# Kernel tuning notes

Measured on AMD Instinct MI355X. Metric: run time of the kernel, lower is better.

## Reference

```python
import jax, jax.numpy as jnp
import numpy as np

N = 524288
H = 128
EPS = 1e-4
SYMP_N = 32  # min(N, 32)
# loss weights from init_kwargs
W_RECON, W_CONS, W_EVO, W_SYMP, W_GAUGE = 1.0, 10.0, 5.0, 0.1, 5.0


def _mlp(x, W1, b1, W2, b2, W3, b3):
    h = jnp.tanh(x @ W1 + b1)
    h = jnp.tanh(h @ W2 + b2)
    return h @ W3 + b3


def _encode(p, q, params):
    out = _mlp(jnp.stack([p, q], axis=-1), *params)  # [N,2]
    return out[:, 0], out[:, 1]


def _decode(P, Q, params):
    out = _mlp(jnp.stack([P, Q], axis=-1), *params)
    return out[:, 0], out[:, 1]


def setup_inputs() -> dict:
    key = jax.random.key(0)
    ks = jax.random.split(key, 24)
    f32 = jnp.float32

    def nrm(k, shape, scale=1.0):
        return (scale * jax.random.normal(k, shape, dtype=f32))

    inp = {
        'p0': nrm(ks[0], (N,)),
        'q0': nrm(ks[1], (N,)),
        'p1': nrm(ks[2], (N,)),
        'q1': nrm(ks[3], (N,)),
        'omega_values': jax.random.uniform(ks[4], (N,), dtype=f32, minval=0.5, maxval=2.0),
        'dt': jnp.asarray(0.05, dtype=f32),
        'P_true': nrm(ks[5], (N,)),
        'Q_true': nrm(ks[6], (N,)),
        # encoder params (2 -> H -> H -> 2), fan-in scaled init
        'enc_W1': nrm(ks[7], (2, H), 1.0 / np.sqrt(2.0)),
        'enc_b1': jnp.zeros((H,), f32),
        'enc_W2': nrm(ks[8], (H, H), 1.0 / np.sqrt(H)),
        'enc_b2': jnp.zeros((H,), f32),
        'enc_W3': nrm(ks[9], (H, 2), 1.0 / np.sqrt(H)),
        'enc_b3': jnp.zeros((2,), f32),
        # decoder params
        'dec_W1': nrm(ks[10], (2, H), 1.0 / np.sqrt(2.0)),
        'dec_b1': jnp.zeros((H,), f32),
        'dec_W2': nrm(ks[11], (H, H), 1.0 / np.sqrt(H)),
        'dec_b2': jnp.zeros((H,), f32),
        'dec_W3': nrm(ks[12], (H, 2), 1.0 / np.sqrt(H)),
        'dec_b3': jnp.zeros((2,), f32),
    }
    return inp


def _loss(p0, q0, p1, q1, omega_values, dt, P_true, Q_true, enc, dec):
    P0, Q0 = _encode(p0, q0, enc)
    P1, Q1 = _encode(p1, q1, enc)
    p0_recon, q0_recon = _decode(P0, Q0, dec)

    recon_loss = jnp.mean((p0 - p0_recon) ** 2 + (q0 - q0_recon) ** 2)
    conservation_loss = jnp.mean((P0 - P1) ** 2)
    evolution_loss = jnp.mean(1.0 - jnp.cos((Q1 - Q0) - omega_values * dt))

    # symplectic loss: batched central finite differences over first 32 samples
    pi, qi = p0[:SYMP_N], q0[:SYMP_N]
    pp = jnp.concatenate([pi + EPS, pi - EPS, pi, pi])          # [4*32]
    qq = jnp.concatenate([qi, qi, qi + EPS, qi - EPS])
    P, Q = _encode(pp, qq, enc)
    P_pp, P_pm, P_qp, P_qm = jnp.split(P, 4)
    Q_pp, Q_pm, Q_qp, Q_qm = jnp.split(Q, 4)
    inv2e = 1.0 / (2.0 * EPS)
    dP_dp = (P_pp - P_pm) * inv2e
    dP_dq = (P_qp - P_qm) * inv2e
    dQ_dp = (Q_pp - Q_pm) * inv2e
    dQ_dq = (Q_qp - Q_qm) * inv2e
    pb = dP_dq * dQ_dp - dP_dp * dQ_dq
    symplectic_loss = jnp.mean((jnp.abs(pb) - 1.0) ** 2)

    gauge_loss = jnp.mean((P0 - P_true) ** 2) + jnp.mean(1.0 - jnp.cos(Q0 - Q_true))

    total = (W_RECON * recon_loss + W_CONS * conservation_loss
             + W_EVO * evolution_loss + W_SYMP * symplectic_loss
             + W_GAUGE * gauge_loss)
    return jnp.stack([total, recon_loss, conservation_loss,
                      evolution_loss, symplectic_loss, gauge_loss])


def reference(p0, q0, p1, q1, omega_values, dt, P_true, Q_true,
              enc_W1, enc_b1, enc_W2, enc_b2, enc_W3, enc_b3,
              dec_W1, dec_b1, dec_W2, dec_b2, dec_W3, dec_b3):
    enc = (enc_W1, enc_b1, enc_W2, enc_b2, enc_W3, enc_b3)
    dec = (dec_W1, dec_b1, dec_W2, dec_b2, dec_W3, dec_b3)
    return _loss(p0, q0, p1, q1, omega_values, dt, P_true, Q_true, enc, dec)
```

## Files before the change

kernel.cpp:

```cpp
#include <hip/hip_runtime.h>
#include <stdint.h>
#include <math.h>


constexpr float EPS_FD = 1e-4f;
constexpr int NBLK = 256;

typedef float f32x4 __attribute__((ext_vector_type(4)));
typedef short s16x8 __attribute__((ext_vector_type(8)));

__device__ __forceinline__ float tanh_fast(float x) {
  float e = __builtin_amdgcn_exp2f(x * 2.8853900817779268f);
  return 1.0f - 2.0f * __builtin_amdgcn_rcpf(e + 1.0f);
}
__device__ __forceinline__ float cos_fast(float x) {
  return __builtin_amdgcn_cosf(x * 0.15915494309189535f);
}
__device__ __forceinline__ unsigned bf16rne(float f) {
  union { float f; unsigned u; } v; v.f = f;
  return (v.u + 0x7FFFu + ((v.u >> 16) & 1u)) >> 16;
}
__device__ __forceinline__ unsigned pack2rne(float a, float b) {
  return bf16rne(a) | (bf16rne(b) << 16);
}
__device__ __forceinline__ unsigned packbf(float lo, float hi) {
  union { float f; unsigned u; } a, b; a.f = lo; b.f = hi;
  return __builtin_amdgcn_perm(b.u + 0x8000u, a.u + 0x8000u, 0x07060302u);
}

template<bool SCAT>
__device__ __forceinline__ void mlp_pass(
    float pe, float qe, unsigned* hrow, const uint4* Bf, const float* epi,
    float w100, float w101, float w110, float w111, float b10, float b11,
    int lane, int quad, int l15, float& vP, float& vQ)
{
#pragma unroll
  for (int ee = 0; ee < 16; ee++) {
    int src = SCAT ? (16 * (ee >> 2) + (ee & 3)) : ee;
    float p = __shfl(pe, src, 64);
    float q = __shfl(qe, src, 64);
    float a0 = tanh_fast(fmaf(p, w100, fmaf(q, w110, b10)));
    float a1 = tanh_fast(fmaf(p, w101, fmaf(q, w111, b11)));
    hrow[ee * 68 + lane] = packbf(a0, a1);
  }
  __builtin_amdgcn_wave_barrier();

  s16x8 A[4];
#pragma unroll
  for (int s = 0; s < 4; s++) {
    uint4 u = *reinterpret_cast<const uint4*>(&hrow[l15 * 68 + 16 * s + 4 * quad]);
    A[s] = *reinterpret_cast<s16x8*>(&u);
  }
  __builtin_amdgcn_wave_barrier();

  f32x4 acc[8];
#pragma unroll
  for (int t = 0; t < 8; t++) {
    float b2v = epi[16 * t + l15];
    f32x4 z = {b2v, b2v, b2v, b2v};
    acc[t] = z;
  }
#pragma unroll
  for (int s = 0; s < 4; s++) {
#pragma unroll
    for (int t = 0; t < 8; t++) {
      uint4 bu = Bf[(s * 8 + t) * 64 + lane];
      s16x8 Bv = *reinterpret_cast<s16x8*>(&bu);
      acc[t] = __builtin_amdgcn_mfma_f32_16x16x32_bf16(A[s], Bv, acc[t], 0, 0, 0);
    }
  }

  float sP[4] = {0, 0, 0, 0}, sQ[4] = {0, 0, 0, 0};
#pragma unroll
  for (int t = 0; t < 8; t++) {
    float w3Pv = epi[128 + 16 * t + l15];
    float w3Qv = epi[256 + 16 * t + l15];
#pragma unroll
    for (int r = 0; r < 4; r++) {
      float h = tanh_fast(acc[t][r]);
      sP[r] = fmaf(h, w3Pv, sP[r]);
      sQ[r] = fmaf(h, w3Qv, sQ[r]);
    }
  }
#pragma unroll
  for (int m = 1; m < 16; m <<= 1) {
#pragma unroll
    for (int r = 0; r < 4; r++) {
      sP[r] += __shfl_xor(sP[r], m, 64);
      sQ[r] += __shfl_xor(sQ[r], m, 64);
    }
  }
  vP = (l15 == 0) ? sP[0] : (l15 == 1) ? sP[1] : (l15 == 2) ? sP[2] : sP[3];
  vQ = (l15 == 0) ? sQ[0] : (l15 == 1) ? sQ[1] : (l15 == 2) ? sQ[2] : sQ[3];
}

__global__ __launch_bounds__(1024, 1) void mlp_main(
    const float* __restrict__ p0, const float* __restrict__ q0,
    const float* __restrict__ p1, const float* __restrict__ q1,
    const float* __restrict__ eW1, const float* __restrict__ eb1,
    const float* __restrict__ eW2, const float* __restrict__ eb2,
    const float* __restrict__ eW3, const float* __restrict__ eb3,
    const float* __restrict__ dW1, const float* __restrict__ db1,
    const float* __restrict__ dW2, const float* __restrict__ db2,
    const float* __restrict__ dW3, const float* __restrict__ db3,
    const float* __restrict__ omega, const float* __restrict__ Pt,
    const float* __restrict__ Qt, const float* __restrict__ dtp,
    float* __restrict__ acc5, unsigned* __restrict__ counter,
    float* __restrict__ PQ, float* __restrict__ out, int n)
{
  __shared__ uint4 BfE[2048];
  __shared__ uint4 BfD[2048];
  __shared__ unsigned h1s[16][16 * 68 + 4];
  __shared__ float encEpi[384];
  __shared__ float decEpi[384];
  __shared__ float red[16][5];
  __shared__ unsigned lastflag;

  int tid = threadIdx.x;
#pragma unroll
  for (int it = 0; it < 8; it++) {
    int id = tid + it * 1024;
    int jj = id & 3, ln = (id >> 2) & 63, f = id >> 8;
    int s = f >> 3, t = f & 7;
    int k   = 32 * s + 8 * (ln >> 4) + 2 * jj;
    int col = 16 * t + (ln & 15);
    ((unsigned*)BfE)[id] = pack2rne(eW2[k * 128 + col], eW2[(k + 1) * 128 + col]);
    ((unsigned*)BfD)[id] = pack2rne(dW2[k * 128 + col], dW2[(k + 1) * 128 + col]);
  }
  if (tid < 128) {
    encEpi[tid]       = eb2[tid];
    encEpi[128 + tid] = eW3[2 * tid];
    encEpi[256 + tid] = eW3[2 * tid + 1];
  } else if (tid < 256) {
    int u = tid - 128;
    decEpi[u]       = db2[u];
    decEpi[128 + u] = dW3[2 * u];
    decEpi[256 + u] = dW3[2 * u + 1];
  }

  int wave = tid >> 6, lane = tid & 63;
  int quad = lane >> 4, l15 = lane & 15;

  float ew100 = eW1[2 * lane],       ew101 = eW1[2 * lane + 1];
  float ew110 = eW1[128 + 2 * lane], ew111 = eW1[128 + 2 * lane + 1];
  float eb10 = eb1[2 * lane], eb11 = eb1[2 * lane + 1];
  float dw100 = dW1[2 * lane],       dw101 = dW1[2 * lane + 1];
  float dw110 = dW1[128 + 2 * lane], dw111 = dW1[128 + 2 * lane + 1];
  float db10 = db1[2 * lane], db11 = db1[2 * lane + 1];
  float eb3P = eb3[0], eb3Q = eb3[1];
  float db3P = db3[0], db3Q = db3[1];
  float dt = dtp[0];
  float s0 = 0.f, s1 = 0.f, s2 = 0.f, s3 = 0.f, s4 = 0.f;
  __syncthreads();

  int nwaves = gridDim.x * 16;
  int gwave  = blockIdx.x * 16 + wave;
  int ntiles = (n + 15) >> 4;
  unsigned* hrow = &h1s[wave][0];

  if (gwave < 128) {
    int r = gwave;
    int m = r & 31, c = r >> 5;
    float p = p0[m], q = q0[m];
    p += (c == 0) ? EPS_FD : (c == 1) ? -EPS_FD : 0.f;
    q += (c == 2) ? EPS_FD : (c == 3) ? -EPS_FD : 0.f;
    float* hf = (float*)hrow;
    int t0 = 2 * lane, t1 = 2 * lane + 1;
    float h0 = tanhf(fmaf(p, eW1[t0], fmaf(q, eW1[128 + t0], eb1[t0])));
    float h1v = tanhf(fmaf(p, eW1[t1], fmaf(q, eW1[128 + t1], eb1[t1])));
    hf[t0] = h0; hf[t1] = h1v;
    __builtin_amdgcn_wave_barrier();
    float a0 = eb2[t0], a1 = eb2[t1];
#pragma unroll 8
    for (int k = 0; k < 128; k++) {
      float hk = hf[k];
      a0 = fmaf(hk, eW2[k * 128 + t0], a0);
      a1 = fmaf(hk, eW2[k * 128 + t1], a1);
    }
    float g0 = tanhf(a0), g1 = tanhf(a1);
    float cP = fmaf(g0, eW3[2 * t0],     g1 * eW3[2 * t1]);
    float cQ = fmaf(g0, eW3[2 * t0 + 1], g1 * eW3[2 * t1 + 1]);
#pragma unroll
    for (int mm = 1; mm < 64; mm <<= 1) {
      cP += __shfl_xor(cP, mm, 64);
      cQ += __shfl_xor(cQ, mm, 64);
    }
    if (lane == 0) {
      atomicExch(&PQ[2 * r],     cP + eb3P);
      atomicExch(&PQ[2 * r + 1], cQ + eb3Q);
    }
    __builtin_amdgcn_wave_barrier();
  }

  for (int tile = gwave; tile < ntiles; tile += nwaves) {
    int base = tile * 16;
    int e = base + l15; if (e >= n) e = n - 1;
    float p0e = p0[e], q0e = q0[e];
    float p1e = p1[e], q1e = q1[e];
    int o = base + quad * 4 + l15;
    int o16 = base + quad * 4 + (l15 & 3);
    if (o16 >= n) o16 = n - 1;
    float Lom = omega[o16], LPt = Pt[o16], LQt = Qt[o16];
    float Lp0 = p0[o16],    Lq0 = q0[o16];

    float P0v, Q0v, P1v, Q1v, RPv, RQv;
    mlp_pass<false>(p0e, q0e, hrow, BfE, encEpi,
                    ew100, ew101, ew110, ew111, eb10, eb11,
                    lane, quad, l15, P0v, Q0v);
    P0v += eb3P; Q0v += eb3Q;
    mlp_pass<false>(p1e, q1e, hrow, BfE, encEpi,
                    ew100, ew101, ew110, ew111, eb10, eb11,
                    lane, quad, l15, P1v, Q1v);
    P1v += eb3P; Q1v += eb3Q;
    mlp_pass<true>(P0v, Q0v, hrow, BfD, decEpi,
                   dw100, dw101, dw110, dw111, db10, db11,
                   lane, quad, l15, RPv, RQv);
    RPv += db3P; RQv += db3Q;

    if (l15 < 4 && o < n) {
      float dp = Lp0 - RPv, dq = Lq0 - RQv;
      s0 += dp * dp + dq * dq;
      float d1 = P0v - P1v; s1 += d1 * d1;
      s2 += 1.0f - cos_fast(Q1v - Q0v - Lom * dt);
      float g = P0v - LPt; s3 += g * g;
      s4 += 1.0f - cos_fast(Q0v - LQt);
    }
  }

#pragma unroll
  for (int m = 1; m < 64; m <<= 1) {
    s0 += __shfl_xor(s0, m, 64);
    s1 += __shfl_xor(s1, m, 64);
    s2 += __shfl_xor(s2, m, 64);
    s3 += __shfl_xor(s3, m, 64);
    s4 += __shfl_xor(s4, m, 64);
  }
  if (lane == 0) {
    red[wave][0] = s0; red[wave][1] = s1; red[wave][2] = s2;
    red[wave][3] = s3; red[wave][4] = s4;
  }
  __syncthreads();
  if (tid == 0) {
#pragma unroll
    for (int i = 0; i < 5; i++) {
      float v = 0.f;
#pragma unroll
      for (int w = 0; w < 16; w++) v += red[w][i];
      atomicAdd(&acc5[i], v);
    }
    __threadfence();
    unsigned prev = atomicAdd(counter, 1u);
    lastflag = (prev == gridDim.x - 1) ? 1u : 0u;
  }
  __syncthreads();
  if (lastflag) {
    __threadfence();
    if (tid < 64) {
      float v = 0.f;
      if (tid < 32) {
        float Ppp = atomicAdd(&PQ[2 * tid], 0.f);
        float Qpp = atomicAdd(&PQ[2 * tid + 1], 0.f);
        float Ppm = atomicAdd(&PQ[2 * (32 + tid)], 0.f);
        float Qpm = atomicAdd(&PQ[2 * (32 + tid) + 1], 0.f);
        float Pqp = atomicAdd(&PQ[2 * (64 + tid)], 0.f);
        float Qqp = atomicAdd(&PQ[2 * (64 + tid) + 1], 0.f);
        float Pqm = atomicAdd(&PQ[2 * (96 + tid)], 0.f);
        float Qqm = atomicAdd(&PQ[2 * (96 + tid) + 1], 0.f);
        float inv2e = 1.0f / (2.0f * EPS_FD);
        float dPdp = (Ppp - Ppm) * inv2e, dPdq = (Pqp - Pqm) * inv2e;
        float dQdp = (Qpp - Qpm) * inv2e, dQdq = (Qqp - Qqm) * inv2e;
        float pb = dPdq * dQdp - dPdp * dQdq;
        float d = fabsf(pb) - 1.0f;
        v = d * d;
      }
#pragma unroll
      for (int m = 1; m < 64; m <<= 1) v += __shfl_xor(v, m, 64);
      if (tid == 0) {
        float inv_n = 1.0f / (float)n;
        float recon = atomicAdd(&acc5[0], 0.f) * inv_n;
        float cons  = atomicAdd(&acc5[1], 0.f) * inv_n;
        float evo   = atomicAdd(&acc5[2], 0.f) * inv_n;
        float gauge = (atomicAdd(&acc5[3], 0.f) + atomicAdd(&acc5[4], 0.f)) * inv_n;
        float symp  = v * (1.0f / 32.0f);
        float total = recon + 10.0f * cons + 5.0f * evo + 0.1f * symp + 5.0f * gauge;
        out[0] = total; out[1] = recon; out[2] = cons;
        out[3] = evo;   out[4] = symp;  out[5] = gauge;
      }
    }
  }
}

extern "C" void kernel_launch(void* const* d_in, const int* in_sizes, int n_in,
                              void* d_out, int out_size, void* d_ws, size_t ws_size,
                              hipStream_t stream)
{
  const float* p0    = (const float*)d_in[0];
  const float* q0    = (const float*)d_in[1];
  const float* p1    = (const float*)d_in[2];
  const float* q1    = (const float*)d_in[3];
  const float* omega = (const float*)d_in[4];
  const float* dtp   = (const float*)d_in[5];
  const float* Pt    = (const float*)d_in[6];
  const float* Qt    = (const float*)d_in[7];
  const float* encW1 = (const float*)d_in[8];
  const float* encb1 = (const float*)d_in[9];
  const float* encW2 = (const float*)d_in[10];
  const float* encb2 = (const float*)d_in[11];
  const float* encW3 = (const float*)d_in[12];
  const float* encb3 = (const float*)d_in[13];
  const float* decW1 = (const float*)d_in[14];
  const float* decb1 = (const float*)d_in[15];
  const float* decW2 = (const float*)d_in[16];
  const float* decb2 = (const float*)d_in[17];
  const float* decW3 = (const float*)d_in[18];
  const float* decb3 = (const float*)d_in[19];

  int n = in_sizes[0];
  float* acc5 = (float*)d_ws;
  unsigned* counter = (unsigned*)(acc5 + 8);
  float* PQ = (float*)(acc5 + 16);

  hipMemsetAsync(acc5, 0, 64, stream);

  mlp_main<<<NBLK, 1024, 0, stream>>>(
      p0, q0, p1, q1,
      encW1, encb1, encW2, encb2, encW3, encb3,
      decW1, decb1, decW2, decb2, decW3, decb3,
      omega, Pt, Qt, dtp, acc5, counter, PQ, (float*)d_out, n);
}
```

Measured before the change: 278.5 us.

## Fuse the two encoder passes to share weight-fragment loads and interleave MFMAs

The two encoder MLP evaluations (p0/q0 and p1/q1) now run together. Each B-weight fragment is loaded once and fed to two independent MFMA chains, and the layer-3 epilogue is done per column tile right after its accumulation. This halves encoder weight-fragment loads and gives the MFMA pipe two independent dependency chains to overlap. It also reduces live accumulators from eight to one or two per tile. The cost is more registers for the second A-fragment set and the extra partial sums, which could affect occupancy or cause spills.

After: 274.2 us. No clear change (-1.6%).

```diff
diff --git a/kernel.cpp b/kernel.cpp
--- a/kernel.cpp
+++ b/kernel.cpp
@@ -29,10 +29,10 @@
 }
 
 template<bool SCAT>
-__device__ __forceinline__ void mlp_pass(
-    float pe, float qe, unsigned* hrow, const uint4* Bf, const float* epi,
+__device__ __forceinline__ void layer1_frags(
+    float pe, float qe, unsigned* hrow,
     float w100, float w101, float w110, float w111, float b10, float b11,
-    int lane, int quad, int l15, float& vP, float& vQ)
+    int lane, int quad, int l15, s16x8 (&A)[4])
 {
 #pragma unroll
   for (int ee = 0; ee < 16; ee++) {
@@ -44,40 +44,91 @@
     hrow[ee * 68 + lane] = packbf(a0, a1);
   }
   __builtin_amdgcn_wave_barrier();
-
-  s16x8 A[4];
 #pragma unroll
   for (int s = 0; s < 4; s++) {
     uint4 u = *reinterpret_cast<const uint4*>(&hrow[l15 * 68 + 16 * s + 4 * quad]);
     A[s] = *reinterpret_cast<s16x8*>(&u);
   }
   __builtin_amdgcn_wave_barrier();
-
-  f32x4 acc[8];
+}
+
+__device__ __forceinline__ void enc_pair(
+    float p0e, float q0e, float p1e, float q1e,
+    unsigned* hrow, const uint4* Bf, const float* epi,
+    float w100, float w101, float w110, float w111, float b10, float b11,
+    int lane, int quad, int l15,
+    float& P0v, float& Q0v, float& P1v, float& Q1v)
+{
+  s16x8 A0[4], A1[4];
+  layer1_frags<false>(p0e, q0e, hrow, w100, w101, w110, w111, b10, b11,
+                      lane, quad, l15, A0);
+  layer1_frags<false>(p1e, q1e, hrow, w100, w101, w110, w111, b10, b11,
+                      lane, quad, l15, A1);
+
+  float sP0[4] = {0,0,0,0}, sQ0[4] = {0,0,0,0};
+  float sP1[4] = {0,0,0,0}, sQ1[4] = {0,0,0,0};
 #pragma unroll
   for (int t = 0; t < 8; t++) {
     float b2v = epi[16 * t + l15];
-    f32x4 z = {b2v, b2v, b2v, b2v};
-    acc[t] = z;
-  }
-#pragma unroll
-  for (int s = 0; s < 4; s++) {
-#pragma unroll
-    for (int t = 0; t < 8; t++) {
+    f32x4 acc0 = {b2v, b2v, b2v, b2v};
+    f32x4 acc1 = {b2v, b2v, b2v, b2v};
+#pragma unroll
+    for (int s = 0; s < 4; s++) {
       uint4 bu = Bf[(s * 8 + t) * 64 + lane];
       s16x8 Bv = *reinterpret_cast<s16x8*>(&bu);
-      acc[t] = __builtin_amdgcn_mfma_f32_16x16x32_bf16(A[s], Bv, acc[t], 0, 0, 0);
-    }
-  }
-
-  float sP[4] = {0, 0, 0, 0}, sQ[4] = {0, 0, 0, 0};
-#pragma unroll
-  for (int t = 0; t < 8; t++) {
+      acc0 = __builtin_amdgcn_mfma_f32_16x16x32_bf16(A0[s], Bv, acc0, 0, 0, 0);
+      acc1 = __builtin_amdgcn_mfma_f32_16x16x32_bf16(A1[s], Bv, acc1, 0, 0, 0);
+    }
     float w3Pv = epi[128 + 16 * t + l15];
     float w3Qv = epi[256 + 16 * t + l15];
 #pragma unroll
     for (int r = 0; r < 4; r++) {
-      float h = tanh_fast(acc[t][r]);
+      float h0 = tanh_fast(acc0[r]);
+      float h1 = tanh_fast(acc1[r]);
+      sP0[r] = fmaf(h0, w3Pv, sP0[r]); sQ0[r] = fmaf(h0, w3Qv, sQ0[r]);
+      sP1[r] = fmaf(h1, w3Pv, sP1[r]); sQ1[r] = fmaf(h1, w3Qv, sQ1[r]);
+    }
+  }
+#pragma unroll
+  for (int m = 1; m < 16; m <<= 1) {
+#pragma unroll
+    for (int r = 0; r < 4; r++) {
+      sP0[r] += __shfl_xor(sP0[r], m, 64);
+      sQ0[r] += __shfl_xor(sQ0[r], m, 64);
+      sP1[r] += __shfl_xor(sP1[r], m, 64);
+      sQ1[r] += __shfl_xor(sQ1[r], m, 64);
+    }
+  }
+  P0v = (l15 == 0) ? sP0[0] : (l15 == 1) ? sP0[1] : (l15 == 2) ? sP0[2] : sP0[3];
+  Q0v = (l15 == 0) ? sQ0[0] : (l15 == 1) ? sQ0[1] : (l15 == 2) ? sQ0[2] : sQ0[3];
+  P1v = (l15 == 0) ? sP1[0] : (l15 == 1) ? sP1[1] : (l15 == 2) ? sP1[2] : sP1[3];
+  Q1v = (l15 == 0) ? sQ1[0] : (l15 == 1) ? sQ1[1] : (l15 == 2) ? sQ1[2] : sQ1[3];
+}
+
+__device__ __forceinline__ void dec_pass(
+    float pe, float qe, unsigned* hrow, const uint4* Bf, const float* epi,
+    float w100, float w101, float w110, float w111, float b10, float b11,
+    int lane, int quad, int l15, float& vP, float& vQ)
+{
+  s16x8 A[4];
+  layer1_frags<true>(pe, qe, hrow, w100, w101, w110, w111, b10, b11,
+                     lane, quad, l15, A);
+  float sP[4] = {0,0,0,0}, sQ[4] = {0,0,0,0};
+#pragma unroll
+  for (int t = 0; t < 8; t++) {
+    float b2v = epi[16 * t + l15];
+    f32x4 acc = {b2v, b2v, b2v, b2v};
+#pragma unroll
+    for (int s = 0; s < 4; s++) {
+      uint4 bu = Bf[(s * 8 + t) * 64 + lane];
+      s16x8 Bv = *reinterpret_cast<s16x8*>(&bu);
+      acc = __builtin_amdgcn_mfma_f32_16x16x32_bf16(A[s], Bv, acc, 0, 0, 0);
+    }
+    float w3Pv = epi[128 + 16 * t + l15];
+    float w3Qv = epi[256 + 16 * t + l15];
+#pragma unroll
+    for (int r = 0; r < 4; r++) {
+      float h = tanh_fast(acc[r]);
       sP[r] = fmaf(h, w3Pv, sP[r]);
       sQ[r] = fmaf(h, w3Qv, sQ[r]);
     }
@@ -204,17 +255,14 @@
     float Lp0 = p0[o16],    Lq0 = q0[o16];
 
     float P0v, Q0v, P1v, Q1v, RPv, RQv;
-    mlp_pass<false>(p0e, q0e, hrow, BfE, encEpi,
-                    ew100, ew101, ew110, ew111, eb10, eb11,
-                    lane, quad, l15, P0v, Q0v);
+    enc_pair(p0e, q0e, p1e, q1e, hrow, BfE, encEpi,
+             ew100, ew101, ew110, ew111, eb10, eb11,
+             lane, quad, l15, P0v, Q0v, P1v, Q1v);
     P0v += eb3P; Q0v += eb3Q;
-    mlp_pass<false>(p1e, q1e, hrow, BfE, encEpi,
-                    ew100, ew101, ew110, ew111, eb10, eb11,
-                    lane, quad, l15, P1v, Q1v);
     P1v += eb3P; Q1v += eb3Q;
-    mlp_pass<true>(P0v, Q0v, hrow, BfD, decEpi,
-                   dw100, dw101, dw110, dw111, db10, db11,
-                   lane, quad, l15, RPv, RQv);
+    dec_pass(P0v, Q0v, hrow, BfD, decEpi,
+             dw100, dw101, dw110, dw111, db10, db11,
+             lane, quad, l15, RPv, RQv);
     RPv += db3P; RQv += db3Q;
 
     if (l15 < 4 && o < n) {
```
